# Kernel tuning notes

Hardware: AMD Instinct MI355X
Metric: run time of the kernel (lower is better)

Reference implementation:

```python
import jax, jax.numpy as jnp
import numpy as np

EMBED_DIM = 1024
NUM_HEADS = 16
HEAD_DIM = EMBED_DIM // NUM_HEADS


def setup_inputs() -> dict:
    key = jax.random.key(0)
    ks = jax.random.split(key, 9)
    B, S, D = 2, 2048, EMBED_DIM
    scale = 1.0 / np.sqrt(D)
    x = jax.random.normal(ks[0], (B, S, D), dtype=jnp.float32)
    Wq = jax.random.normal(ks[1], (D, D), dtype=jnp.float32) * scale
    Wk = jax.random.normal(ks[2], (D, D), dtype=jnp.float32) * scale
    Wv = jax.random.normal(ks[3], (D, D), dtype=jnp.float32) * scale
    Wo = jax.random.normal(ks[4], (D, D), dtype=jnp.float32) * scale
    bq = jnp.zeros((D,), jnp.float32)
    bk = jnp.zeros((D,), jnp.float32)
    bv = jnp.zeros((D,), jnp.float32)
    bo = jnp.zeros((D,), jnp.float32)
    return {"x": x, "Wq": Wq, "bq": bq, "Wk": Wk, "bk": bk,
            "Wv": Wv, "bv": bv, "Wo": Wo, "bo": bo}


def reference(x, Wq, bq, Wk, bk, Wv, bv, Wo, bo):
    B, S, D = x.shape
    H, Dh = NUM_HEADS, HEAD_DIM
    # QKV projections -> [B, H, S, Dh]
    q = (x @ Wq + bq).reshape(B, S, H, Dh).transpose(0, 2, 1, 3)
    k = (x @ Wk + bk).reshape(B, S, H, Dh).transpose(0, 2, 1, 3)
    v = (x @ Wv + bv).reshape(B, S, H, Dh).transpose(0, 2, 1, 3)
    # scores [B, H, S, S], scaled by sqrt(head_dim)
    scores = jnp.einsum('bhqd,bhkd->bhqk', q, k) / jnp.sqrt(jnp.float32(Dh))
    attn = jax.nn.softmax(scores, axis=-1)
    out = jnp.einsum('bhqk,bhkd->bhqd', attn, v)  # [B, H, S, Dh]
    out = out.transpose(0, 2, 1, 3).reshape(B, S, D)
    return out @ Wo + bo
```

## Files before the change

kernel.cpp:

```cpp
#include <hip/hip_runtime.h>
#include <hip/hip_bf16.h>

typedef short bf16x8 __attribute__((ext_vector_type(8)));
typedef float f32x4 __attribute__((ext_vector_type(4)));
typedef unsigned uint2v __attribute__((ext_vector_type(2)));

#define MFMA16(a, b, c) __builtin_amdgcn_mfma_f32_16x16x32_bf16((a), (b), (c), 0, 0, 0)

#if __has_builtin(__builtin_amdgcn_exp2f)
#define EXP2(x) __builtin_amdgcn_exp2f(x)
#else
#define EXP2(x) exp2f(x)
#endif

static constexpr int B_ = 2, S_ = 2048, D_ = 1024, H_ = 16, DH = 64;
static constexpr int M_ = B_ * S_;
static constexpr int K_ = D_;
static constexpr float kQS = 0.18033688011112042f;

static __device__ __forceinline__ ushort f2bf(float f) {
    __hip_bfloat16 h = __float2bfloat16(f);
    return *reinterpret_cast<ushort*>(&h);
}

static __device__ __forceinline__ void gload16(const ushort* g, ushort* l) {
    __builtin_amdgcn_global_load_lds((const __attribute__((address_space(1))) void*)g,
                                     (__attribute__((address_space(3))) void*)l, 16, 0, 0);
}

static __device__ __forceinline__ unsigned pkbf(float lo, float hi) {
    return __builtin_amdgcn_perm(__builtin_bit_cast(unsigned, hi),
                                 __builtin_bit_cast(unsigned, lo), 0x07060302u);
}

__global__ __launch_bounds__(256) void cvt_f2b(const float* __restrict__ in,
                                               ushort* __restrict__ out) {
    int i = blockIdx.x * blockDim.x + threadIdx.x;
    float4 v = reinterpret_cast<const float4*>(in)[i];
    ushort4 o;
    o.x = f2bf(v.x); o.y = f2bf(v.y); o.z = f2bf(v.z); o.w = f2bf(v.w);
    reinterpret_cast<ushort4*>(out)[i] = o;
}

__global__ __launch_bounds__(256) void transpose_w4(const float* __restrict__ W0,
                                                    const float* __restrict__ W1,
                                                    const float* __restrict__ W2,
                                                    const float* __restrict__ W3,
                                                    ushort* __restrict__ T0,
                                                    ushort* __restrict__ T1,
                                                    ushort* __restrict__ T2,
                                                    ushort* __restrict__ T3) {
    __shared__ float tile[32][33];
    int z = blockIdx.z;
    const float* W = (z == 0) ? W0 : (z == 1) ? W1 : (z == 2) ? W2 : W3;
    ushort* T = (z == 0) ? T0 : (z == 1) ? T1 : (z == 2) ? T2 : T3;
    float sc = (z == 0) ? kQS : 1.0f;
    int bx = blockIdx.x, by = blockIdx.y;
    int tx = threadIdx.x, ty = threadIdx.y;
#pragma unroll
    for (int i = 0; i < 4; i++)
        tile[ty + i * 8][tx] = W[(by * 32 + ty + i * 8) * D_ + bx * 32 + tx];
    __syncthreads();
#pragma unroll
    for (int i = 0; i < 4; i++)
        T[(bx * 32 + ty + i * 8) * K_ + by * 32 + tx] = f2bf(tile[tx][ty + i * 8] * sc);
}

template <int MODE, int TN>
__global__ __launch_bounds__(256, 3) void gemm128(const ushort* __restrict__ A,
                                                  const ushort* __restrict__ Wt,
                                                  const float* __restrict__ bias_q,
                                                  const float* __restrict__ bias_k,
                                                  const float* __restrict__ bias_v,
                                                  ushort* __restrict__ Qb,
                                                  ushort* __restrict__ Kb,
                                                  ushort* __restrict__ Vtb,
                                                  float* __restrict__ outf) {
    constexpr int NJ = TN / 32;
    __shared__ __align__(16) ushort As[128 * 32];
    __shared__ __align__(16) ushort Bs[TN * 32];

    int m0 = blockIdx.x * 128;
    int n0 = blockIdx.y * TN;
    int t = threadIdx.x;
    int lane = t & 63, w = t >> 6;
    int ln = lane & 15, lq = lane >> 4;
    int wm = (w >> 1) * 64, wn = (w & 1) * (TN / 2);

    int c0 = t, c1 = t + 256;
    const ushort* Ag0 = A + (size_t)(m0 + (c0 >> 2)) * K_ + (c0 & 3) * 8;
    const ushort* Ag1 = A + (size_t)(m0 + (c1 >> 2)) * K_ + (c1 & 3) * 8;
    const ushort* Bg0 = Wt + (size_t)(n0 + (c0 >> 2)) * K_ + (c0 & 3) * 8;
    const ushort* Bg1 = Wt + (size_t)(n0 + (c1 >> 2)) * K_ + (c1 & 3) * 8;
    ushort* Al0 = As + c0 * 8;
    ushort* Al1 = As + c1 * 8;
    ushort* Bl0 = Bs + c0 * 8;
    ushort* Bl1 = Bs + c1 * 8;

    f32x4 acc[4][NJ];
#pragma unroll
    for (int i = 0; i < 4; i++)
#pragma unroll
        for (int j = 0; j < NJ; j++) acc[i][j] = f32x4{0.f, 0.f, 0.f, 0.f};

    for (int k0 = 0; k0 < K_; k0 += 32) {
        gload16(Ag0 + k0, Al0);
        gload16(Ag1 + k0, Al1);
        gload16(Bg0 + k0, Bl0);
        if (TN == 128) gload16(Bg1 + k0, Bl1);
        __syncthreads();
        bf16x8 af[4], bfr[NJ];
#pragma unroll
        for (int i = 0; i < 4; i++)
            af[i] = *reinterpret_cast<const bf16x8*>(As + (wm + i * 16 + ln) * 32 + lq * 8);
#pragma unroll
        for (int j = 0; j < NJ; j++)
            bfr[j] = *reinterpret_cast<const bf16x8*>(Bs + (wn + j * 16 + ln) * 32 + lq * 8);
#pragma unroll
        for (int i = 0; i < 4; i++)
#pragma unroll
            for (int j = 0; j < NJ; j++)
                acc[i][j] = MFMA16(af[i], bfr[j], acc[i][j]);
        __syncthreads();
    }

#pragma unroll
    for (int j = 0; j < NJ; j++) {
        int n = n0 + wn + j * 16 + ln;
        if (MODE == 1) {
            float bv = bias_q[n];
#pragma unroll
            for (int i = 0; i < 4; i++) {
#pragma unroll
                for (int r = 0; r < 4; r++) {
                    int m = m0 + wm + i * 16 + lq * 4 + r;
                    outf[(size_t)m * D_ + n] = acc[i][j][r] + bv;
                }
            }
        } else {
            int which = n >> 10, nn = n & 1023, h = nn >> 6, dh = nn & 63;
            const float* bp = (which == 0) ? bias_q : (which == 1) ? bias_k : bias_v;
            float bv = bp[nn];
            if (which == 0) bv *= kQS;
            if (which == 2) {
#pragma unroll
                for (int i = 0; i < 4; i++) {
                    int m = m0 + wm + i * 16 + lq * 4;
                    int b = m >> 11, s0 = m & 2047;
                    ushort4 o4;
                    o4.x = f2bf(acc[i][j][0] + bv);
                    o4.y = f2bf(acc[i][j][1] + bv);
                    o4.z = f2bf(acc[i][j][2] + bv);
                    o4.w = f2bf(acc[i][j][3] + bv);
                    *reinterpret_cast<ushort4*>(Vtb + (((size_t)(b * H_ + h) * DH) + dh) * S_ + s0) = o4;
                }
            } else {
                ushort* dst = (which == 0) ? Qb : Kb;
#pragma unroll
                for (int i = 0; i < 4; i++) {
#pragma unroll
                    for (int r = 0; r < 4; r++) {
                        int m = m0 + wm + i * 16 + lq * 4 + r;
                        int b = m >> 11, s = m & 2047;
                        dst[(((b * H_ + h) * S_) + s) * DH + dh] = f2bf(acc[i][j][r] + bv);
                    }
                }
            }
        }
    }
}

__global__ __launch_bounds__(256) void attn64t(const ushort* __restrict__ Q,
                                               const ushort* __restrict__ K,
                                               const ushort* __restrict__ Vt,
                                               ushort* __restrict__ O) {
    __shared__ __align__(16) ushort Kl[512 * 8];
    __shared__ __align__(16) ushort Vl[512 * 8];
    __shared__ __align__(16) ushort Pl[4][16 * 72];

    int bid = blockIdx.x;
    int qb = bid & 31;
    int bh = bid >> 5;
    int t = threadIdx.x;
    int lane = t & 63, w = t >> 6;
    int ln = lane & 15, lq = lane >> 4;
    int qt = qb * 4 + w;

    const ushort* Qp = Q + (size_t)bh * S_ * DH;
    const ushort* Kp = K + (size_t)bh * S_ * DH;
    const ushort* Vp = Vt + (size_t)bh * DH * S_;

    bf16x8 qf0 = *reinterpret_cast<const bf16x8*>(Qp + (qt * 16 + ln) * DH + lq * 8);
    bf16x8 qf1 = *reinterpret_cast<const bf16x8*>(Qp + (qt * 16 + ln) * DH + 32 + lq * 8);

    bf16x8 ones;
#pragma unroll
    for (int j = 0; j < 8; j++) ones[j] = (short)0x3F80;

    int c0 = t, c1 = t + 256;
    const ushort* Kg0 = Kp + (size_t)(c0 & 63) * DH + (c0 >> 6) * 8;
    const ushort* Kg1 = Kp + (size_t)(c1 & 63) * DH + (c1 >> 6) * 8;
    const ushort* Vg0 = Vp + (size_t)(c0 & 63) * S_ + (c0 >> 6) * 8;
    const ushort* Vg1 = Vp + (size_t)(c1 & 63) * S_ + (c1 >> 6) * 8;
    ushort* Kl0 = Kl + c0 * 8;
    ushort* Kl1 = Kl + c1 * 8;
    ushort* Vl0 = Vl + c0 * 8;
    ushort* Vl1 = Vl + c1 * 8;

    f32x4 o_acc[4];
    f32x4 l_acc = {0.f, 0.f, 0.f, 0.f};
#pragma unroll
    for (int nt = 0; nt < 4; nt++) o_acc[nt] = f32x4{0.f, 0.f, 0.f, 0.f};

    for (int kt = 0; kt < S_ / 64; kt++) {
        int kb = kt * 64;
        gload16(Kg0 + (size_t)kb * DH, Kl0);
        gload16(Kg1 + (size_t)kb * DH, Kl1);
        gload16(Vg0 + kb, Vl0);
        gload16(Vg1 + kb, Vl1);
        __syncthreads();

        f32x4 sc[4];
#pragma unroll
        for (int nt = 0; nt < 4; nt++) {
            bf16x8 kf0 = *reinterpret_cast<const bf16x8*>(Kl + (lq * 64 + nt * 16 + ln) * 8);
            bf16x8 kf1 = *reinterpret_cast<const bf16x8*>(Kl + ((4 + lq) * 64 + nt * 16 + ln) * 8);
            f32x4 c = {0.f, 0.f, 0.f, 0.f};
            c = MFMA16(kf0, qf0, c);
            c = MFMA16(kf1, qf1, c);
            sc[nt] = c;
        }
#pragma unroll
        for (int nt = 0; nt < 4; nt++) {
            float p0 = EXP2(sc[nt][0]);
            float p1 = EXP2(sc[nt][1]);
            float p2 = EXP2(sc[nt][2]);
            float p3 = EXP2(sc[nt][3]);
            uint2v pk;
            pk.x = pkbf(p0, p1);
            pk.y = pkbf(p2, p3);
            *reinterpret_cast<uint2v*>(&Pl[w][ln * 72 + nt * 16 + lq * 4]) = pk;
        }
        bf16x8 pf0 = *reinterpret_cast<const bf16x8*>(&Pl[w][ln * 72 + lq * 8]);
        bf16x8 pf1 = *reinterpret_cast<const bf16x8*>(&Pl[w][ln * 72 + 32 + lq * 8]);
        l_acc = MFMA16(pf0, ones, l_acc);
        l_acc = MFMA16(pf1, ones, l_acc);
#pragma unroll
        for (int nt = 0; nt < 4; nt++) {
            bf16x8 vf0 = *reinterpret_cast<const bf16x8*>(Vl + (lq * 64 + nt * 16 + ln) * 8);
            bf16x8 vf1 = *reinterpret_cast<const bf16x8*>(Vl + ((4 + lq) * 64 + nt * 16 + ln) * 8);
            o_acc[nt] = MFMA16(pf0, vf0, o_acc[nt]);
            o_acc[nt] = MFMA16(pf1, vf1, o_acc[nt]);
        }
        __syncthreads();
    }

    float linv[4];
#pragma unroll
    for (int r = 0; r < 4; r++) linv[r] = 1.0f / l_acc[r];
    int b = bh >> 4, h = bh & 15;
#pragma unroll
    for (int nt = 0; nt < 4; nt++)
#pragma unroll
        for (int r = 0; r < 4; r++) {
            int s = qt * 16 + lq * 4 + r;
            O[((b * S_ + s) * H_ + h) * DH + nt * 16 + ln] =
                f2bf(o_acc[nt][r] * linv[r]);
        }
}

extern "C" void kernel_launch(void* const* d_in, const int* in_sizes, int n_in,
                              void* d_out, int out_size, void* d_ws, size_t ws_size,
                              hipStream_t stream) {
    const float* x  = (const float*)d_in[0];
    const float* Wq = (const float*)d_in[1];
    const float* bq = (const float*)d_in[2];
    const float* Wk = (const float*)d_in[3];
    const float* bk = (const float*)d_in[4];
    const float* Wv = (const float*)d_in[5];
    const float* bv = (const float*)d_in[6];
    const float* Wo = (const float*)d_in[7];
    const float* bo = (const float*)d_in[8];
    float* out = (float*)d_out;

    char* ws = (char*)d_ws;
    const size_t MB = 1024 * 1024;
    ushort* wtq = (ushort*)(ws + 0 * MB);
    ushort* wtk = (ushort*)(ws + 2 * MB);
    ushort* wtv = (ushort*)(ws + 4 * MB);
    ushort* wto = (ushort*)(ws + 6 * MB);
    ushort* xb  = (ushort*)(ws + 8 * MB);
    ushort* Qb  = (ushort*)(ws + 16 * MB);
    ushort* Kb  = (ushort*)(ws + 24 * MB);
    ushort* Vtb = (ushort*)(ws + 32 * MB);
    ushort* AO  = (ushort*)(ws + 40 * MB);

    cvt_f2b<<<(M_ * K_ / 4) / 256, 256, 0, stream>>>(x, xb);

    transpose_w4<<<dim3(32, 32, 4), dim3(32, 8), 0, stream>>>(
        Wq, Wk, Wv, Wo, wtq, wtk, wtv, wto);

    gemm128<0, 128><<<dim3(M_ / 128, 3072 / 128), 256, 0, stream>>>(
        xb, wtq, bq, bk, bv, Qb, Kb, Vtb, nullptr);

    attn64t<<<32 * 32, 256, 0, stream>>>(Qb, Kb, Vtb, AO);

    gemm128<1, 64><<<dim3(M_ / 128, D_ / 64), 256, 0, stream>>>(
        AO, wto, bo, nullptr, nullptr, nullptr, nullptr, nullptr, out);
}
```

Baseline: 204.4 us.

## Double-buffer GEMM LDS tiles and fuse input conversion into weight transpose

The projection GEMM now keeps two LDS buffers per operand. It issues the next K-tile's global-to-LDS loads right after a single barrier, so those loads overlap the MFMA work on the current tile, and one of the two barriers per iteration is dropped. The separate x fp32-to-bf16 conversion kernel is folded into the weight transpose launch as an extra grid slice, which saves one launch. The cost is twice the LDS per block, which could reduce occupancy.

```diff
diff --git a/kernel.cpp b/kernel.cpp
--- a/kernel.cpp
+++ b/kernel.cpp
@@ -33,30 +33,36 @@
                                  __builtin_bit_cast(unsigned, lo), 0x07060302u);
 }
 
-__global__ __launch_bounds__(256) void cvt_f2b(const float* __restrict__ in,
-                                               ushort* __restrict__ out) {
-    int i = blockIdx.x * blockDim.x + threadIdx.x;
-    float4 v = reinterpret_cast<const float4*>(in)[i];
-    ushort4 o;
-    o.x = f2bf(v.x); o.y = f2bf(v.y); o.z = f2bf(v.z); o.w = f2bf(v.w);
-    reinterpret_cast<ushort4*>(out)[i] = o;
-}
-
-__global__ __launch_bounds__(256) void transpose_w4(const float* __restrict__ W0,
-                                                    const float* __restrict__ W1,
-                                                    const float* __restrict__ W2,
-                                                    const float* __restrict__ W3,
-                                                    ushort* __restrict__ T0,
-                                                    ushort* __restrict__ T1,
-                                                    ushort* __restrict__ T2,
-                                                    ushort* __restrict__ T3) {
+__global__ __launch_bounds__(256) void prep5(const float* __restrict__ x,
+                                             const float* __restrict__ W0,
+                                             const float* __restrict__ W1,
+                                             const float* __restrict__ W2,
+                                             const float* __restrict__ W3,
+                                             ushort* __restrict__ xb,
+                                             ushort* __restrict__ T0,
+                                             ushort* __restrict__ T1,
+                                             ushort* __restrict__ T2,
+                                             ushort* __restrict__ T3) {
+    int z = blockIdx.z;
+    int tx = threadIdx.x, ty = threadIdx.y;
+    int t = ty * 32 + tx;
+    if (z == 4) {
+        int blk = blockIdx.y * 32 + blockIdx.x;
+#pragma unroll
+        for (int k = 0; k < 4; k++) {
+            int i = blk * 1024 + k * 256 + t;
+            float4 v = reinterpret_cast<const float4*>(x)[i];
+            ushort4 o;
+            o.x = f2bf(v.x); o.y = f2bf(v.y); o.z = f2bf(v.z); o.w = f2bf(v.w);
+            reinterpret_cast<ushort4*>(xb)[i] = o;
+        }
+        return;
+    }
     __shared__ float tile[32][33];
-    int z = blockIdx.z;
     const float* W = (z == 0) ? W0 : (z == 1) ? W1 : (z == 2) ? W2 : W3;
     ushort* T = (z == 0) ? T0 : (z == 1) ? T1 : (z == 2) ? T2 : T3;
     float sc = (z == 0) ? kQS : 1.0f;
     int bx = blockIdx.x, by = blockIdx.y;
-    int tx = threadIdx.x, ty = threadIdx.y;
 #pragma unroll
     for (int i = 0; i < 4; i++)
         tile[ty + i * 8][tx] = W[(by * 32 + ty + i * 8) * D_ + bx * 32 + tx];
@@ -77,8 +83,8 @@
                                                   ushort* __restrict__ Vtb,
                                                   float* __restrict__ outf) {
     constexpr int NJ = TN / 32;
-    __shared__ __align__(16) ushort As[128 * 32];
-    __shared__ __align__(16) ushort Bs[TN * 32];
+    __shared__ __align__(16) ushort As[2][128 * 32];
+    __shared__ __align__(16) ushort Bs[2][TN * 32];
 
     int m0 = blockIdx.x * 128;
     int n0 = blockIdx.y * TN;
@@ -92,10 +98,6 @@
     const ushort* Ag1 = A + (size_t)(m0 + (c1 >> 2)) * K_ + (c1 & 3) * 8;
     const ushort* Bg0 = Wt + (size_t)(n0 + (c0 >> 2)) * K_ + (c0 & 3) * 8;
     const ushort* Bg1 = Wt + (size_t)(n0 + (c1 >> 2)) * K_ + (c1 & 3) * 8;
-    ushort* Al0 = As + c0 * 8;
-    ushort* Al1 = As + c1 * 8;
-    ushort* Bl0 = Bs + c0 * 8;
-    ushort* Bl1 = Bs + c1 * 8;
 
     f32x4 acc[4][NJ];
 #pragma unroll
@@ -103,25 +105,33 @@
 #pragma unroll
         for (int j = 0; j < NJ; j++) acc[i][j] = f32x4{0.f, 0.f, 0.f, 0.f};
 
-    for (int k0 = 0; k0 < K_; k0 += 32) {
-        gload16(Ag0 + k0, Al0);
-        gload16(Ag1 + k0, Al1);
-        gload16(Bg0 + k0, Bl0);
-        if (TN == 128) gload16(Bg1 + k0, Bl1);
+    gload16(Ag0, As[0] + c0 * 8);
+    gload16(Ag1, As[0] + c1 * 8);
+    gload16(Bg0, Bs[0] + c0 * 8);
+    if (TN == 128) gload16(Bg1, Bs[0] + c1 * 8);
+
+    for (int kt = 0; kt < K_ / 32; kt++) {
         __syncthreads();
+        int cur = kt & 1;
+        if (kt + 1 < K_ / 32) {
+            int k0 = (kt + 1) * 32;
+            gload16(Ag0 + k0, As[cur ^ 1] + c0 * 8);
+            gload16(Ag1 + k0, As[cur ^ 1] + c1 * 8);
+            gload16(Bg0 + k0, Bs[cur ^ 1] + c0 * 8);
+            if (TN == 128) gload16(Bg1 + k0, Bs[cur ^ 1] + c1 * 8);
+        }
         bf16x8 af[4], bfr[NJ];
 #pragma unroll
         for (int i = 0; i < 4; i++)
-            af[i] = *reinterpret_cast<const bf16x8*>(As + (wm + i * 16 + ln) * 32 + lq * 8);
+            af[i] = *reinterpret_cast<const bf16x8*>(As[cur] + (wm + i * 16 + ln) * 32 + lq * 8);
 #pragma unroll
         for (int j = 0; j < NJ; j++)
-            bfr[j] = *reinterpret_cast<const bf16x8*>(Bs + (wn + j * 16 + ln) * 32 + lq * 8);
+            bfr[j] = *reinterpret_cast<const bf16x8*>(Bs[cur] + (wn + j * 16 + ln) * 32 + lq * 8);
 #pragma unroll
         for (int i = 0; i < 4; i++)
 #pragma unroll
             for (int j = 0; j < NJ; j++)
                 acc[i][j] = MFMA16(af[i], bfr[j], acc[i][j]);
-        __syncthreads();
     }
 
 #pragma unroll
@@ -295,10 +305,8 @@
     ushort* Vtb = (ushort*)(ws + 32 * MB);
     ushort* AO  = (ushort*)(ws + 40 * MB);
 
-    cvt_f2b<<<(M_ * K_ / 4) / 256, 256, 0, stream>>>(x, xb);
-
-    transpose_w4<<<dim3(32, 32, 4), dim3(32, 8), 0, stream>>>(
-        Wq, Wk, Wv, Wo, wtq, wtk, wtv, wto);
+    prep5<<<dim3(32, 32, 5), dim3(32, 8), 0, stream>>>(
+        x, Wq, Wk, Wv, Wo, xb, wtq, wtk, wtv, wto);
 
     gemm128<0, 128><<<dim3(M_ / 128, 3072 / 128), 256, 0, stream>>>(
         xb, wtq, bq, bk, bv, Qb, Kb, Vtb, nullptr);
```

Result: no change. 206.8 us (+1.2%).
